# Kernel optimization log

Measured on AMD Instinct MI355X. Metric: run time of the kernel, lower is better.

## Reference

```python
import jax, jax.numpy as jnp
import numpy as np

SAMPLE_RATE = 44100
NUM_FILTERS = 3
FREQ_LO, FREQ_HI = 100.0, 3000.0
Q_LO, Q_HI = 1.0, 5.0
GAIN_LO, GAIN_HI = -24.0, 24.0


def _center_freqs():
    # power_ratio(i/N, f_lo, f_hi) = f_lo * (f_hi/f_lo)**(i/N)
    return [FREQ_LO * (FREQ_HI / FREQ_LO) ** (i / NUM_FILTERS) for i in range(NUM_FILTERS)]


def setup_inputs() -> dict:
    key = jax.random.key(0)
    k1, k2, k3 = jax.random.split(key, 3)
    audio = jax.random.normal(k1, (32, 441000), dtype=jnp.float32)  # [B, T]
    # Q sampled like power_ratio(u, q_lo, q_hi) = q_lo*(q_hi/q_lo)**u
    u = jax.random.uniform(k2, (NUM_FILTERS,), dtype=jnp.float32)
    qs = Q_LO * (Q_HI / Q_LO) ** u
    gains = jax.random.uniform(k3, (NUM_FILTERS,), dtype=jnp.float32,
                               minval=GAIN_LO, maxval=GAIN_HI)
    return {"audio": audio, "qs": qs, "gains": gains}


def _biquad(x, b0, b1, b2, a1, a2):
    """Direct-form-I biquad over time axis. x: [B, T]; coeffs normalized by a0."""
    B = x.shape[0]
    z = jnp.zeros((B,), x.dtype)

    def step(carry, xn):
        x1, x2, y1, y2 = carry
        yn = b0 * xn + b1 * x1 + b2 * x2 - a1 * y1 - a2 * y2
        return (xn, x1, yn, y1), yn

    _, y = jax.lax.scan(step, (z, z, z, z), x.T)  # scan over T
    return y.T


def _peaking_eq(audio, center_freq, gain, Q):
    # torchaudio.functional.equalizer_biquad coefficients
    w0 = 2.0 * jnp.pi * center_freq / SAMPLE_RATE
    alpha = jnp.sin(w0) / (2.0 * Q)
    A = jnp.exp(gain / 40.0 * jnp.log(10.0))  # 10**(gain/40)
    b0 = 1.0 + alpha * A
    b1 = -2.0 * jnp.cos(w0)
    b2 = 1.0 - alpha * A
    a0 = 1.0 + alpha / A
    a1 = -2.0 * jnp.cos(w0)
    a2 = 1.0 - alpha / A
    return _biquad(audio, b0 / a0, b1 / a0, b2 / a0, a1 / a0, a2 / a0)


def reference(audio, qs, gains):
    cfs = _center_freqs()
    for i in range(NUM_FILTERS):
        audio = _peaking_eq(audio, cfs[i], gains[i], qs[i])
    return audio
```

## Files before the change

### kernel.cpp

```cpp
#include <hip/hip_runtime.h>
#include <math.h>

#define SR      44100.0
#define T_LEN   441000
#define B_ROWS  32
#define NCH     13782
#define GCH     (B_ROWS * NCH)
#define WPR     216
#define NWAVE   (B_ROWS * WPR)
#define NBLK    (NWAVE / 4)
#define NSEG    8
#define SEGCH   1724
#define ROUNDS  10

#define WS_MAT  0
#define WS_T    512
#define WS_F    4096

typedef __attribute__((address_space(1))) const void gconst_t;
typedef __attribute__((address_space(3))) void lds_t;
#define GL2LDS(gp, lp) __builtin_amdgcn_global_load_lds((gconst_t*)(gp), (lds_t*)(lp), 16, 0, 0)


#define COMPUTE_COEFS_TO_LDS(scoef, qs, gains) do { \
    if (threadIdx.x < 3) { \
      int f = threadIdx.x; \
      double cfq = 100.0 * exp(log(30.0) * (double)f / 3.0); \
      double w0 = 2.0 * M_PI * cfq / SR; \
      double alpha = sin(w0) / (2.0 * (double)qs[f]); \
      double Ag = exp((double)gains[f] * (2.302585092994045684 / 40.0)); \
      double a0 = 1.0 + alpha / Ag; \
      scoef[f*5+0] = (float)((1.0 + alpha * Ag) / a0); \
      scoef[f*5+1] = (float)((-2.0 * cos(w0)) / a0); \
      scoef[f*5+2] = (float)((1.0 - alpha * Ag) / a0); \
      scoef[f*5+3] = (float)((-2.0 * cos(w0)) / a0); \
      scoef[f*5+4] = (float)((1.0 - alpha / Ag) / a0); \
    } \
  } while (0)

#define LOAD_COEFS(cf) \
  const float b00=cf[0],b10=cf[1],b20=cf[2],a10=cf[3],a20=cf[4]; \
  const float b01=cf[5],b11=cf[6],b21=cf[7],a11=cf[8],a21=cf[9]; \
  const float b02=cf[10],b12=cf[11],b22=cf[12],a12=cf[13],a22=cf[14];

#define CASCADE_STEP(xx) do { \
    float y1 = fmaf(b00, (xx), s11); \
    s11 = fmaf(-a10, y1, fmaf(b10, (xx), s21)); \
    s21 = fmaf(-a20, y1, b20 * (xx)); \
    float y2 = fmaf(b01, y1, s12); \
    s12 = fmaf(-a11, y2, fmaf(b11, y1, s22)); \
    s22 = fmaf(-a21, y2, b21 * y1); \
    y3 = fmaf(b02, y2, s13); \
    s13 = fmaf(-a12, y3, fmaf(b12, y2, s23)); \
    s23 = fmaf(-a22, y3, b22 * y2); \
  } while (0)

#define MV6(dst, M, v, add) do { \
    _Pragma("unroll") \
    for (int _i = 0; _i < 6; _i++) { \
      float _s = (add)[_i]; \
      _Pragma("unroll") \
      for (int _k = 0; _k < 6; _k++) _s = fmaf((M)[_i*6+_k], (v)[_k], _s); \
      (dst)[_i] = _s; \
    } \
  } while (0)

__device__ __forceinline__ void mm6d(const double* X, const double* Y, double* Z, int t) {
  if (t < 36) {
    int i = t / 6, j = t % 6;
    double s = 0.0;
    #pragma unroll
    for (int k = 0; k < 6; k++) s += X[i*6+k] * Y[k*6+j];
    Z[t] = s;
  }
}


__global__ __launch_bounds__(256) void kA_states(const float* __restrict__ x,
                                                 const float* __restrict__ qs,
                                                 const float* __restrict__ gains,
                                                 float* __restrict__ ws) {
  __shared__ float lds[4 * 2048];
  __shared__ float scoef[16];
  int wib = threadIdx.x >> 6, lane = threadIdx.x & 63;
  int gw = blockIdx.x * 4 + wib;
  int row = gw / WPR, wci = gw % WPR;
  long rowbase = (long)row * T_LEN;
  int s0 = wci << 11;
  int span4 = (min(2048, T_LEN - s0)) >> 2;
  const float4* xp = (const float4*)(x + rowbase + s0);
  float* slab = lds + (wib << 11);
  if (span4 == 512) {
    #pragma unroll
    for (int i = 0; i < 8; i++) {
      int s = (i << 6) + lane;
      int g = (s & ~7) | ((s & 7) ^ ((s >> 3) & 7));
      GL2LDS(xp + g, slab + (i << 8));
    }
  } else {
    #pragma unroll
    for (int i = 0; i < 8; i++) {
      int s = (i << 6) + lane;
      int g = (s & ~7) | ((s & 7) ^ ((s >> 3) & 7));
      if (g < span4) GL2LDS(xp + g, slab + (i << 8));
    }
  }
  COMPUTE_COEFS_TO_LDS(scoef, qs, gains);
  __syncthreads();
  int ci = (wci << 6) + lane;
  if (ci < NCH) {
    LOAD_COEFS(scoef);
    int rem = min(32, T_LEN - (ci << 5));
    int n4 = rem >> 2;
    const float* rowp = slab + (lane << 5);
    int xr = lane & 7;
    float s11=0,s21=0,s12=0,s22=0,s13=0,s23=0, y3;
    if (n4 == 8) {
      #pragma unroll
      for (int j4 = 0; j4 < 8; j4++) {
        float4 v = *(const float4*)(rowp + ((j4 ^ xr) << 2));
        CASCADE_STEP(v.x); CASCADE_STEP(v.y); CASCADE_STEP(v.z); CASCADE_STEP(v.w);
      }
    } else {
      for (int j4 = 0; j4 < n4; j4++) {
        float4 v = *(const float4*)(rowp + ((j4 ^ xr) << 2));
        CASCADE_STEP(v.x); CASCADE_STEP(v.y); CASCADE_STEP(v.z); CASCADE_STEP(v.w);
      }
    }
    (void)y3;
    float2* F = (float2*)(ws + WS_F + ((long)row * NCH + ci) * 6);
    F[0] = make_float2(s11, s21); F[1] = make_float2(s12, s22); F[2] = make_float2(s13, s23);
  }
}


__device__ __forceinline__ void scan_setup(const float* qs, const float* gains, int t,
                                           double* Da, double* Db, double* Dc, double* Dd,
                                           float* sW, float (*sV)[36], float* sG) {
  __shared__ double dco[3][5];
  if (t < 3) {
    int f = t;
    double cfq = 100.0 * exp(log(30.0) * (double)f / 3.0);
    double w0 = 2.0 * M_PI * cfq / SR;
    double alpha = sin(w0) / (2.0 * (double)qs[f]);
    double Ag = exp((double)gains[f] * (2.302585092994045684 / 40.0));
    double a0 = 1.0 + alpha / Ag;
    dco[f][0] = (1.0 + alpha * Ag) / a0;
    dco[f][1] = (-2.0 * cos(w0)) / a0;
    dco[f][2] = (1.0 - alpha * Ag) / a0;
    dco[f][3] = (-2.0 * cos(w0)) / a0;
    dco[f][4] = (1.0 - alpha / Ag) / a0;
  }
  __syncthreads();
  if (t == 0) {
    double u[7] = {0,0,0,0,0,0,1};
    for (int f = 0; f < 3; f++) {
      double b0=dco[f][0], b1=dco[f][1], b2=dco[f][2], a1=dco[f][3], a2=dco[f][4];
      double yv[7], s1p[7], s2p[7];
      for (int i = 0; i < 7; i++) {
        yv[i]  = b0 * u[i] + ((i == 2*f)   ? 1.0 : 0.0);
        s1p[i] = b1 * u[i] + ((i == 2*f+1) ? 1.0 : 0.0) - a1 * yv[i];
        s2p[i] = b2 * u[i] - a2 * yv[i];
      }
      for (int i = 0; i < 6; i++) { Da[(2*f)*6+i] = s1p[i]; Da[(2*f+1)*6+i] = s2p[i]; }
      for (int i = 0; i < 7; i++) u[i] = yv[i];
    }
  }
  if (t < 36) Dc[t] = (t % 7 == 0) ? 1.0 : 0.0;
  __syncthreads();
  mm6d(Da, Da, Db, t); __syncthreads();
  mm6d(Db, Db, Da, t); __syncthreads();
  mm6d(Da, Da, Db, t); __syncthreads();
  mm6d(Db, Db, Da, t); __syncthreads();
  mm6d(Da, Da, Db, t); __syncthreads();
  if (t < 36) sW[t] = (float)Db[t];
  mm6d(Db, Db, Da, t); __syncthreads();
  double* cur = Da; double* oth = Db;
  double* Gc = Dc; double* Gd = Dd;
  #pragma unroll
  for (int k = 0; k < ROUNDS; k++) {
    if (t < 36) sV[k][t] = (float)cur[t];
    if ((SEGCH >> (k + 1)) & 1) {
      __syncthreads();
      mm6d(Gc, cur, Gd, t); __syncthreads();
      double* tm = Gc; Gc = Gd; Gd = tm;
    }
    if (k < ROUNDS - 1) {
      __syncthreads();
      mm6d(cur, cur, oth, t); __syncthreads();
      double* tm = cur; cur = oth; oth = tm;
    }
  }
  if (t < 36) sG[t] = (float)Gc[t];
  __syncthreads();
}


__global__ __launch_bounds__(1024) void kB_scan(const float* __restrict__ qs,
                                                const float* __restrict__ gains,
                                                float* __restrict__ ws) {
  int seg = blockIdx.x & 7, row = blockIdx.x >> 3, t = threadIdx.x;
  __shared__ double Da[36], Db[36], Dc[36], Dd[36];
  __shared__ float sW[36], sV[ROUNDS][36], sG[36];
  __shared__ float bufA[1024][7], bufB[1024][7];
  scan_setup(qs, gains, t, Da, Db, Dc, Dd, sW, sV, sG);
  if (blockIdx.x == 0 && t < 36) {
    ws[WS_MAT + t] = sW[t];
    #pragma unroll
    for (int k = 0; k < ROUNDS; k++) ws[WS_MAT + (k + 1) * 36 + t] = sV[k][t];
    ws[WS_MAT + 11 * 36 + t] = sG[t];
  }
  int segstart = seg * SEGCH;
  int nch = min(SEGCH, NCH - segstart);
  int nact = nch >> 1;
  float* F = ws + WS_F + ((long)row * NCH + segstart) * 6;
  float v[6] = {0,0,0,0,0,0};
  float f0[6] = {0,0,0,0,0,0};
  if (t < nact) {
    const float4* Fp = (const float4*)(F + 12 * t);
    float4 l0 = Fp[0], l1 = Fp[1], l2 = Fp[2];
    f0[0]=l0.x; f0[1]=l0.y; f0[2]=l0.z; f0[3]=l0.w; f0[4]=l1.x; f0[5]=l1.y;
    float f1[6] = {l1.z, l1.w, l2.x, l2.y, l2.z, l2.w};
    MV6(v, sW, f0, f1);
  }
  #pragma unroll
  for (int i = 0; i < 6; i++) bufA[t][i] = v[i];
  __syncthreads();
  float (*src)[7] = bufA, (*dst)[7] = bufB;
  for (int k = 0; k < ROUNDS; k++) {
    int d = 1 << k;
    float nv[6];
    if (t >= d) { MV6(nv, sV[k], src[t-d], src[t]); }
    else {
      #pragma unroll
      for (int i = 0; i < 6; i++) nv[i] = src[t][i];
    }
    #pragma unroll
    for (int i = 0; i < 6; i++) dst[t][i] = nv[i];
    __syncthreads();
    float (*tm)[7] = src; src = dst; dst = tm;
  }
  if (t == nact - 1) {
    float* Tp = ws + WS_T + (long)blockIdx.x * 6;
    #pragma unroll
    for (int i = 0; i < 6; i++) Tp[i] = src[t][i];
  }
  if (t < nact) {
    float e[6];
    if (t > 0) {
      #pragma unroll
      for (int i = 0; i < 6; i++) e[i] = src[t-1][i];
    } else {
      #pragma unroll
      for (int i = 0; i < 6; i++) e[i] = 0.0f;
    }
    float e1[6];
    MV6(e1, sW, e, f0);
    float4* Fp = (float4*)(F + 12 * t);
    Fp[0] = make_float4(e[0], e[1], e[2], e[3]);
    Fp[1] = make_float4(e[4], e[5], e1[0], e1[1]);
    Fp[2] = make_float4(e1[2], e1[3], e1[4], e1[5]);
  }
}


__global__ __launch_bounds__(256) void kC_emit(const float* __restrict__ x,
                                               const float* __restrict__ qs,
                                               const float* __restrict__ gains,
                                               float* __restrict__ y,
                                               const float* __restrict__ ws) {
  __shared__ float lds[4 * 2048];
  __shared__ float scoef[16];
  __shared__ float smat[432];
  __shared__ float sTT[96];
  __shared__ float sO[96];
  int tid = threadIdx.x;
  int wib = tid >> 6, lane = tid & 63;
  int gw = blockIdx.x * 4 + wib;
  int row = gw / WPR, wci = gw % WPR;
  int rowA = (blockIdx.x * 4) / WPR;
  long rowbase = (long)row * T_LEN;
  int s0 = wci << 11;
  int span4 = (min(2048, T_LEN - s0)) >> 2;
  const float4* xp = (const float4*)(x + rowbase + s0);
  float* slab = lds + (wib << 11);
  if (span4 == 512) {
    #pragma unroll
    for (int i = 0; i < 8; i++) {
      int s = (i << 6) + lane;
      int g = (s & ~7) | ((s & 7) ^ ((s >> 3) & 7));
      GL2LDS(xp + g, slab + (i << 8));
    }
  } else {
    #pragma unroll
    for (int i = 0; i < 8; i++) {
      int s = (i << 6) + lane;
      int g = (s & ~7) | ((s & 7) ^ ((s >> 3) & 7));
      if (g < span4) GL2LDS(xp + g, slab + (i << 8));
    }
  }
  for (int i = tid; i < 432; i += 256) smat[i] = ws[WS_MAT + i];
  {
    int rowB = (blockIdx.x * 4 + 3) / WPR;
    if (tid < 96) {
      int r = (tid < 48) ? rowA : rowB;
      int j = tid - ((tid < 48) ? 0 : 48);
      sTT[tid] = ws[WS_T + (long)r * 48 + j];
    }
  }
  COMPUTE_COEFS_TO_LDS(scoef, qs, gains);
  int ci = (wci << 6) + lane;
  float e0=0,e1v=0,e2=0,e3=0,e4=0,e5=0;
  if (ci < NCH) {
    const float2* E = (const float2*)(ws + WS_F + ((long)row * NCH + ci) * 6);
    float2 p0 = E[0], p1 = E[1], p2 = E[2];
    e0=p0.x; e1v=p0.y; e2=p1.x; e3=p1.y; e4=p2.x; e5=p2.y;
  }
  __syncthreads();
  if (tid < 16) {
    int rsel = tid >> 3, sg = tid & 7;
    const float* Gm = smat + 11 * 36;
    float o[6] = {0,0,0,0,0,0};
    for (int s2 = 0; s2 < sg; s2++) {
      float no[6];
      MV6(no, Gm, o, &sTT[rsel * 48 + s2 * 6]);
      #pragma unroll
      for (int i = 0; i < 6; i++) o[i] = no[i];
    }
    #pragma unroll
    for (int i = 0; i < 6; i++) sO[tid * 6 + i] = o[i];
  }
  __syncthreads();
  if (ci < NCH) {
    LOAD_COEFS(scoef);
    int seg = ci / SEGCH;
    int d = ci - seg * SEGCH;
    int rsel = (row == rowA) ? 0 : 1;
    const float* op = sO + (rsel * 8 + seg) * 6;
    float m[6];
    #pragma unroll
    for (int i = 0; i < 6; i++) m[i] = op[i];
    float z6[6] = {0,0,0,0,0,0};
    #pragma unroll
    for (int k = 0; k < 11; k++) {
      if ((d >> k) & 1) {
        float nm[6];
        MV6(nm, smat + k * 36, m, z6);
        #pragma unroll
        for (int i = 0; i < 6; i++) m[i] = nm[i];
      }
    }
    float s11=e0+m[0], s21=e1v+m[1], s12=e2+m[2], s22=e3+m[3], s13=e4+m[4], s23=e5+m[5];
    int rem = min(32, T_LEN - (ci << 5));
    int n4 = rem >> 2;
    float* rowp = slab + (lane << 5);
    int xr = lane & 7;
    float y3;
    if (n4 == 8) {
      #pragma unroll
      for (int j4 = 0; j4 < 8; j4++) {
        float* p = rowp + ((j4 ^ xr) << 2);
        float4 v = *(const float4*)p;
        float4 o;
        CASCADE_STEP(v.x); o.x = y3;
        CASCADE_STEP(v.y); o.y = y3;
        CASCADE_STEP(v.z); o.z = y3;
        CASCADE_STEP(v.w); o.w = y3;
        *(float4*)p = o;
      }
    } else {
      for (int j4 = 0; j4 < n4; j4++) {
        float* p = rowp + ((j4 ^ xr) << 2);
        float4 v = *(const float4*)p;
        float4 o;
        CASCADE_STEP(v.x); o.x = y3;
        CASCADE_STEP(v.y); o.y = y3;
        CASCADE_STEP(v.z); o.z = y3;
        CASCADE_STEP(v.w); o.w = y3;
        *(float4*)p = o;
      }
    }
  }
  __syncthreads();
  float4* yp = (float4*)(y + rowbase + s0);
  if (span4 == 512) {
    #pragma unroll
    for (int i = 0; i < 8; i++) {
      int g = (i << 6) + lane;
      int s = (g & ~7) | ((g & 7) ^ ((g >> 3) & 7));
      yp[g] = *(const float4*)(slab + (s << 2));
    }
  } else {
    #pragma unroll
    for (int i = 0; i < 8; i++) {
      int g = (i << 6) + lane;
      int s = (g & ~7) | ((g & 7) ^ ((g >> 3) & 7));
      if (g < span4) yp[g] = *(const float4*)(slab + (s << 2));
    }
  }
}

extern "C" void kernel_launch(void* const* d_in, const int* in_sizes, int n_in,
                              void* d_out, int out_size, void* d_ws, size_t ws_size,
                              hipStream_t stream) {
  const float* audio = (const float*)d_in[0];
  const float* qs    = (const float*)d_in[1];
  const float* gains = (const float*)d_in[2];
  float* out = (float*)d_out;
  float* ws  = (float*)d_ws;

  hipLaunchKernelGGL(kA_states, dim3(NBLK), dim3(256), 0, stream, audio, qs, gains, ws);
  hipLaunchKernelGGL(kB_scan, dim3(B_ROWS * NSEG), dim3(1024), 0, stream, qs, gains, ws);
  hipLaunchKernelGGL(kC_emit, dim3(NBLK), dim3(256), 0, stream, audio, qs, gains, out, ws);
}
```

Measured before the change: 68.08 us.

## Fuse intra-block state scan into first kernel, shrink middle scan to per-block offsets

The first kernel now computes the transition-matrix powers itself and runs a 256-chunk Kogge-Stone scan of per-chunk states in LDS, writing exclusive prefixes plus block aggregates. The middle kernel shrinks from 256 blocks of 1024 threads scanning 8 segments per row to 32 tiny blocks scanning 54 block aggregates. The emit kernel then applies only a block offset and up to 8 matrix powers instead of a serial segment chain and 11 powers. This is meant to cut the heavy middle launch and its global state traffic. In exchange, every first-kernel block redoes the double-precision matrix squaring and adds several barriers.

```diff
diff --git a/kernel.cpp b/kernel.cpp
--- a/kernel.cpp
+++ b/kernel.cpp
@@ -6,23 +6,21 @@
 #define B_ROWS  32
 #define NCH     13782
 #define GCH     (B_ROWS * NCH)
-#define WPR     216
-#define NWAVE   (B_ROWS * WPR)
-#define NBLK    (NWAVE / 4)
-#define NSEG    8
-#define SEGCH   1724
-#define ROUNDS  10
+#define BPR     54
+#define NBLK    (B_ROWS * BPR)
+#define NMAT    14
 
 #define WS_MAT  0
-#define WS_T    512
-#define WS_F    4096
+#define WS_AG   512
+#define WS_O    10880
+#define WS_F    21248
 
 typedef __attribute__((address_space(1))) const void gconst_t;
 typedef __attribute__((address_space(3))) void lds_t;
 #define GL2LDS(gp, lp) __builtin_amdgcn_global_load_lds((gconst_t*)(gp), (lds_t*)(lp), 16, 0, 0)
 
 
-#define COMPUTE_COEFS_TO_LDS(scoef, qs, gains) do { \
+#define COMPUTE_COEFS(scoef, dco, qs, gains) do { \
     if (threadIdx.x < 3) { \
       int f = threadIdx.x; \
       double cfq = 100.0 * exp(log(30.0) * (double)f / 3.0); \
@@ -30,11 +28,15 @@
       double alpha = sin(w0) / (2.0 * (double)qs[f]); \
       double Ag = exp((double)gains[f] * (2.302585092994045684 / 40.0)); \
       double a0 = 1.0 + alpha / Ag; \
-      scoef[f*5+0] = (float)((1.0 + alpha * Ag) / a0); \
-      scoef[f*5+1] = (float)((-2.0 * cos(w0)) / a0); \
-      scoef[f*5+2] = (float)((1.0 - alpha * Ag) / a0); \
-      scoef[f*5+3] = (float)((-2.0 * cos(w0)) / a0); \
-      scoef[f*5+4] = (float)((1.0 - alpha / Ag) / a0); \
+      double c0 = (1.0 + alpha * Ag) / a0; \
+      double c1 = (-2.0 * cos(w0)) / a0; \
+      double c2 = (1.0 - alpha * Ag) / a0; \
+      double c3 = c1; \
+      double c4 = (1.0 - alpha / Ag) / a0; \
+      if (dco) { double* dc = (double*)(dco); \
+        dc[f*5+0]=c0; dc[f*5+1]=c1; dc[f*5+2]=c2; dc[f*5+3]=c3; dc[f*5+4]=c4; } \
+      scoef[f*5+0]=(float)c0; scoef[f*5+1]=(float)c1; scoef[f*5+2]=(float)c2; \
+      scoef[f*5+3]=(float)c3; scoef[f*5+4]=(float)c4; \
     } \
   } while (0)
 
@@ -76,15 +78,21 @@
 }
 
 
-__global__ __launch_bounds__(256) void kA_states(const float* __restrict__ x,
-                                                 const float* __restrict__ qs,
-                                                 const float* __restrict__ gains,
-                                                 float* __restrict__ ws) {
-  __shared__ float lds[4 * 2048];
+
+__global__ __launch_bounds__(256) void kA_scan(const float* __restrict__ x,
+                                               const float* __restrict__ qs,
+                                               const float* __restrict__ gains,
+                                               float* __restrict__ ws) {
+  __shared__ __align__(16) float lds[4 * 2048];
+  __shared__ double Da[36], Db[36];
+  __shared__ double dco[15];
+  __shared__ float sVm[NMAT][36];
   __shared__ float scoef[16];
-  int wib = threadIdx.x >> 6, lane = threadIdx.x & 63;
-  int gw = blockIdx.x * 4 + wib;
-  int row = gw / WPR, wci = gw % WPR;
+  const int tid = threadIdx.x;
+  const int wib = tid >> 6, lane = tid & 63;
+  const int b = blockIdx.x;
+  const int row = b / BPR, jb = b - row * BPR;
+  const int wci = (jb << 2) + wib;
   long rowbase = (long)row * T_LEN;
   int s0 = wci << 11;
   int span4 = (min(2048, T_LEN - s0)) >> 2;
@@ -105,10 +113,47 @@
       if (g < span4) GL2LDS(xp + g, slab + (i << 8));
     }
   }
-  COMPUTE_COEFS_TO_LDS(scoef, qs, gains);
-  __syncthreads();
-  int ci = (wci << 6) + lane;
-  if (ci < NCH) {
+  COMPUTE_COEFS(scoef, dco, qs, gains);
+  if (wib == 0) {
+    if (lane == 0) {
+      double u[7] = {0,0,0,0,0,0,1};
+      for (int f = 0; f < 3; f++) {
+        double c0=dco[f*5+0], c1=dco[f*5+1], c2=dco[f*5+2], c3=dco[f*5+3], c4=dco[f*5+4];
+        double yv[7], s1p[7], s2p[7];
+        for (int i = 0; i < 7; i++) {
+          yv[i]  = c0 * u[i] + ((i == 2*f)   ? 1.0 : 0.0);
+          s1p[i] = c1 * u[i] + ((i == 2*f+1) ? 1.0 : 0.0) - c3 * yv[i];
+          s2p[i] = c2 * u[i] - c4 * yv[i];
+        }
+        for (int i = 0; i < 6; i++) { Da[(2*f)*6+i] = s1p[i]; Da[(2*f+1)*6+i] = s2p[i]; }
+        for (int i = 0; i < 7; i++) u[i] = yv[i];
+      }
+    }
+    double* cur = Da; double* oth = Db;
+    #pragma unroll
+    for (int s = 0; s < 5; s++) {
+      mm6d(cur, cur, oth, lane);
+      double* tm = cur; cur = oth; oth = tm;
+    }
+    #pragma unroll
+    for (int k = 0; k < NMAT; k++) {
+      if (lane < 36) {
+        float wv = (float)cur[lane];
+        sVm[k][lane] = wv;
+        if (b == 0) ws[WS_MAT + k*36 + lane] = wv;
+      }
+      if (k < NMAT - 1) {
+        mm6d(cur, cur, oth, lane);
+        double* tm = cur; cur = oth; oth = tm;
+      }
+    }
+  }
+  __syncthreads();
+
+  int ci = (jb << 8) + tid;
+  bool valid = ci < NCH;
+  float f[6] = {0,0,0,0,0,0};
+  if (valid) {
     LOAD_COEFS(scoef);
     int rem = min(32, T_LEN - (ci << 5));
     int n4 = rem >> 2;
@@ -128,138 +173,86 @@
       }
     }
     (void)y3;
-    float2* F = (float2*)(ws + WS_F + ((long)row * NCH + ci) * 6);
-    F[0] = make_float2(s11, s21); F[1] = make_float2(s12, s22); F[2] = make_float2(s13, s23);
-  }
-}
-
-
-__device__ __forceinline__ void scan_setup(const float* qs, const float* gains, int t,
-                                           double* Da, double* Db, double* Dc, double* Dd,
-                                           float* sW, float (*sV)[36], float* sG) {
-  __shared__ double dco[3][5];
-  if (t < 3) {
-    int f = t;
-    double cfq = 100.0 * exp(log(30.0) * (double)f / 3.0);
-    double w0 = 2.0 * M_PI * cfq / SR;
-    double alpha = sin(w0) / (2.0 * (double)qs[f]);
-    double Ag = exp((double)gains[f] * (2.302585092994045684 / 40.0));
-    double a0 = 1.0 + alpha / Ag;
-    dco[f][0] = (1.0 + alpha * Ag) / a0;
-    dco[f][1] = (-2.0 * cos(w0)) / a0;
-    dco[f][2] = (1.0 - alpha * Ag) / a0;
-    dco[f][3] = (-2.0 * cos(w0)) / a0;
-    dco[f][4] = (1.0 - alpha / Ag) / a0;
-  }
-  __syncthreads();
-  if (t == 0) {
-    double u[7] = {0,0,0,0,0,0,1};
-    for (int f = 0; f < 3; f++) {
-      double b0=dco[f][0], b1=dco[f][1], b2=dco[f][2], a1=dco[f][3], a2=dco[f][4];
-      double yv[7], s1p[7], s2p[7];
-      for (int i = 0; i < 7; i++) {
-        yv[i]  = b0 * u[i] + ((i == 2*f)   ? 1.0 : 0.0);
-        s1p[i] = b1 * u[i] + ((i == 2*f+1) ? 1.0 : 0.0) - a1 * yv[i];
-        s2p[i] = b2 * u[i] - a2 * yv[i];
-      }
-      for (int i = 0; i < 6; i++) { Da[(2*f)*6+i] = s1p[i]; Da[(2*f+1)*6+i] = s2p[i]; }
-      for (int i = 0; i < 7; i++) u[i] = yv[i];
-    }
-  }
-  if (t < 36) Dc[t] = (t % 7 == 0) ? 1.0 : 0.0;
-  __syncthreads();
-  mm6d(Da, Da, Db, t); __syncthreads();
-  mm6d(Db, Db, Da, t); __syncthreads();
-  mm6d(Da, Da, Db, t); __syncthreads();
-  mm6d(Db, Db, Da, t); __syncthreads();
-  mm6d(Da, Da, Db, t); __syncthreads();
-  if (t < 36) sW[t] = (float)Db[t];
-  mm6d(Db, Db, Da, t); __syncthreads();
-  double* cur = Da; double* oth = Db;
-  double* Gc = Dc; double* Gd = Dd;
+    f[0]=s11; f[1]=s21; f[2]=s12; f[3]=s22; f[4]=s13; f[5]=s23;
+  }
+  __syncthreads();
+
+  float* src = lds;
+  float* dst = lds + 1792;
   #pragma unroll
-  for (int k = 0; k < ROUNDS; k++) {
-    if (t < 36) sV[k][t] = (float)cur[t];
-    if ((SEGCH >> (k + 1)) & 1) {
-      __syncthreads();
-      mm6d(Gc, cur, Gd, t); __syncthreads();
-      double* tm = Gc; Gc = Gd; Gd = tm;
-    }
-    if (k < ROUNDS - 1) {
-      __syncthreads();
-      mm6d(cur, cur, oth, t); __syncthreads();
-      double* tm = cur; cur = oth; oth = tm;
-    }
-  }
-  if (t < 36) sG[t] = (float)Gc[t];
-  __syncthreads();
-}
-
-
-__global__ __launch_bounds__(1024) void kB_scan(const float* __restrict__ qs,
-                                                const float* __restrict__ gains,
-                                                float* __restrict__ ws) {
-  int seg = blockIdx.x & 7, row = blockIdx.x >> 3, t = threadIdx.x;
-  __shared__ double Da[36], Db[36], Dc[36], Dd[36];
-  __shared__ float sW[36], sV[ROUNDS][36], sG[36];
-  __shared__ float bufA[1024][7], bufB[1024][7];
-  scan_setup(qs, gains, t, Da, Db, Dc, Dd, sW, sV, sG);
-  if (blockIdx.x == 0 && t < 36) {
-    ws[WS_MAT + t] = sW[t];
-    #pragma unroll
-    for (int k = 0; k < ROUNDS; k++) ws[WS_MAT + (k + 1) * 36 + t] = sV[k][t];
-    ws[WS_MAT + 11 * 36 + t] = sG[t];
-  }
-  int segstart = seg * SEGCH;
-  int nch = min(SEGCH, NCH - segstart);
-  int nact = nch >> 1;
-  float* F = ws + WS_F + ((long)row * NCH + segstart) * 6;
-  float v[6] = {0,0,0,0,0,0};
-  float f0[6] = {0,0,0,0,0,0};
-  if (t < nact) {
-    const float4* Fp = (const float4*)(F + 12 * t);
-    float4 l0 = Fp[0], l1 = Fp[1], l2 = Fp[2];
-    f0[0]=l0.x; f0[1]=l0.y; f0[2]=l0.z; f0[3]=l0.w; f0[4]=l1.x; f0[5]=l1.y;
-    float f1[6] = {l1.z, l1.w, l2.x, l2.y, l2.z, l2.w};
-    MV6(v, sW, f0, f1);
-  }
-  #pragma unroll
-  for (int i = 0; i < 6; i++) bufA[t][i] = v[i];
-  __syncthreads();
-  float (*src)[7] = bufA, (*dst)[7] = bufB;
-  for (int k = 0; k < ROUNDS; k++) {
+  for (int i = 0; i < 6; i++) src[tid*7 + i] = f[i];
+  __syncthreads();
+  for (int k = 0; k < 8; k++) {
     int d = 1 << k;
     float nv[6];
-    if (t >= d) { MV6(nv, sV[k], src[t-d], src[t]); }
+    if (tid >= d) { MV6(nv, sVm[k], src + (tid-d)*7, src + tid*7); }
     else {
       #pragma unroll
-      for (int i = 0; i < 6; i++) nv[i] = src[t][i];
-    }
-    #pragma unroll
-    for (int i = 0; i < 6; i++) dst[t][i] = nv[i];
+      for (int i = 0; i < 6; i++) nv[i] = src[tid*7 + i];
+    }
+    #pragma unroll
+    for (int i = 0; i < 6; i++) dst[tid*7 + i] = nv[i];
     __syncthreads();
-    float (*tm)[7] = src; src = dst; dst = tm;
-  }
-  if (t == nact - 1) {
-    float* Tp = ws + WS_T + (long)blockIdx.x * 6;
-    #pragma unroll
-    for (int i = 0; i < 6; i++) Tp[i] = src[t][i];
-  }
-  if (t < nact) {
+    float* tm = src; src = dst; dst = tm;
+  }
+  if (valid) {
     float e[6];
-    if (t > 0) {
-      #pragma unroll
-      for (int i = 0; i < 6; i++) e[i] = src[t-1][i];
+    if (tid > 0) {
+      #pragma unroll
+      for (int i = 0; i < 6; i++) e[i] = src[(tid-1)*7 + i];
     } else {
       #pragma unroll
       for (int i = 0; i < 6; i++) e[i] = 0.0f;
     }
-    float e1[6];
-    MV6(e1, sW, e, f0);
-    float4* Fp = (float4*)(F + 12 * t);
-    Fp[0] = make_float4(e[0], e[1], e[2], e[3]);
-    Fp[1] = make_float4(e[4], e[5], e1[0], e1[1]);
-    Fp[2] = make_float4(e1[2], e1[3], e1[4], e1[5]);
+    float2* E = (float2*)(ws + WS_F + ((long)row * NCH + ci) * 6);
+    E[0] = make_float2(e[0], e[1]); E[1] = make_float2(e[2], e[3]); E[2] = make_float2(e[4], e[5]);
+  }
+  if (tid == 255 && jb < BPR - 1) {
+    #pragma unroll
+    for (int i = 0; i < 6; i++) ws[WS_AG + ((long)row * BPR + jb) * 6 + i] = src[255*7 + i];
+  }
+}
+
+
+__global__ __launch_bounds__(64) void kB_off(float* __restrict__ ws) {
+  int row = blockIdx.x, j = threadIdx.x;
+  __shared__ float sB[6][36];
+  __shared__ float buf[2][64][7];
+  for (int i = j; i < 216; i += 64) sB[i/36][i%36] = ws[WS_MAT + (8 + i/36)*36 + (i%36)];
+  float v[6] = {0,0,0,0,0,0};
+  if (j < BPR - 1) {
+    #pragma unroll
+    for (int i = 0; i < 6; i++) v[i] = ws[WS_AG + ((long)row * BPR + j) * 6 + i];
+  }
+  __syncthreads();
+  #pragma unroll
+  for (int i = 0; i < 6; i++) buf[0][j][i] = v[i];
+  __syncthreads();
+  int cur = 0;
+  for (int k = 0; k < 6; k++) {
+    int d = 1 << k;
+    float nv[6];
+    if (j >= d) { MV6(nv, sB[k], buf[cur][j-d], buf[cur][j]); }
+    else {
+      #pragma unroll
+      for (int i = 0; i < 6; i++) nv[i] = buf[cur][j][i];
+    }
+    #pragma unroll
+    for (int i = 0; i < 6; i++) buf[cur^1][j][i] = nv[i];
+    __syncthreads();
+    cur ^= 1;
+  }
+  if (j < BPR) {
+    float o[6];
+    if (j > 0) {
+      #pragma unroll
+      for (int i = 0; i < 6; i++) o[i] = buf[cur][j-1][i];
+    } else {
+      #pragma unroll
+      for (int i = 0; i < 6; i++) o[i] = 0.0f;
+    }
+    #pragma unroll
+    for (int i = 0; i < 6; i++) ws[WS_O + ((long)row * BPR + j) * 6 + i] = o[i];
   }
 }
 
@@ -269,16 +262,14 @@
                                                const float* __restrict__ gains,
                                                float* __restrict__ y,
                                                const float* __restrict__ ws) {
-  __shared__ float lds[4 * 2048];
+  __shared__ __align__(16) float lds[4 * 2048];
   __shared__ float scoef[16];
-  __shared__ float smat[432];
-  __shared__ float sTT[96];
-  __shared__ float sO[96];
-  int tid = threadIdx.x;
-  int wib = tid >> 6, lane = tid & 63;
-  int gw = blockIdx.x * 4 + wib;
-  int row = gw / WPR, wci = gw % WPR;
-  int rowA = (blockIdx.x * 4) / WPR;
+  __shared__ float smat[288];
+  const int tid = threadIdx.x;
+  const int wib = tid >> 6, lane = tid & 63;
+  const int b = blockIdx.x;
+  const int row = b / BPR, jb = b - row * BPR;
+  const int wci = (jb << 2) + wib;
   long rowbase = (long)row * T_LEN;
   int s0 = wci << 11;
   int span4 = (min(2048, T_LEN - s0)) >> 2;
@@ -299,53 +290,34 @@
       if (g < span4) GL2LDS(xp + g, slab + (i << 8));
     }
   }
-  for (int i = tid; i < 432; i += 256) smat[i] = ws[WS_MAT + i];
+  for (int i = tid; i < 288; i += 256) smat[i] = ws[WS_MAT + i];
+  COMPUTE_COEFS(scoef, (double*)nullptr, qs, gains);
+  float o6[6];
   {
-    int rowB = (blockIdx.x * 4 + 3) / WPR;
-    if (tid < 96) {
-      int r = (tid < 48) ? rowA : rowB;
-      int j = tid - ((tid < 48) ? 0 : 48);
-      sTT[tid] = ws[WS_T + (long)r * 48 + j];
-    }
-  }
-  COMPUTE_COEFS_TO_LDS(scoef, qs, gains);
-  int ci = (wci << 6) + lane;
+    const float* Op = ws + WS_O + ((long)row * BPR + jb) * 6;
+    #pragma unroll
+    for (int i = 0; i < 6; i++) o6[i] = Op[i];
+  }
+  int ci = (jb << 8) + tid;
+  bool valid = ci < NCH;
   float e0=0,e1v=0,e2=0,e3=0,e4=0,e5=0;
-  if (ci < NCH) {
+  if (valid) {
     const float2* E = (const float2*)(ws + WS_F + ((long)row * NCH + ci) * 6);
     float2 p0 = E[0], p1 = E[1], p2 = E[2];
     e0=p0.x; e1v=p0.y; e2=p1.x; e3=p1.y; e4=p2.x; e5=p2.y;
   }
   __syncthreads();
-  if (tid < 16) {
-    int rsel = tid >> 3, sg = tid & 7;
-    const float* Gm = smat + 11 * 36;
-    float o[6] = {0,0,0,0,0,0};
-    for (int s2 = 0; s2 < sg; s2++) {
-      float no[6];
-      MV6(no, Gm, o, &sTT[rsel * 48 + s2 * 6]);
-      #pragma unroll
-      for (int i = 0; i < 6; i++) o[i] = no[i];
-    }
-    #pragma unroll
-    for (int i = 0; i < 6; i++) sO[tid * 6 + i] = o[i];
-  }
-  __syncthreads();
-  if (ci < NCH) {
+  if (valid) {
     LOAD_COEFS(scoef);
-    int seg = ci / SEGCH;
-    int d = ci - seg * SEGCH;
-    int rsel = (row == rowA) ? 0 : 1;
-    const float* op = sO + (rsel * 8 + seg) * 6;
     float m[6];
     #pragma unroll
-    for (int i = 0; i < 6; i++) m[i] = op[i];
+    for (int i = 0; i < 6; i++) m[i] = o6[i];
     float z6[6] = {0,0,0,0,0,0};
     #pragma unroll
-    for (int k = 0; k < 11; k++) {
-      if ((d >> k) & 1) {
+    for (int k = 0; k < 8; k++) {
+      if ((tid >> k) & 1) {
         float nm[6];
-        MV6(nm, smat + k * 36, m, z6);
+        MV6(nm, smat + k*36, m, z6);
         #pragma unroll
         for (int i = 0; i < 6; i++) m[i] = nm[i];
       }
@@ -409,7 +381,7 @@
   float* out = (float*)d_out;
   float* ws  = (float*)d_ws;
 
-  hipLaunchKernelGGL(kA_states, dim3(NBLK), dim3(256), 0, stream, audio, qs, gains, ws);
-  hipLaunchKernelGGL(kB_scan, dim3(B_ROWS * NSEG), dim3(1024), 0, stream, qs, gains, ws);
+  hipLaunchKernelGGL(kA_scan, dim3(NBLK), dim3(256), 0, stream, audio, qs, gains, ws);
+  hipLaunchKernelGGL(kB_off, dim3(B_ROWS), dim3(64), 0, stream, ws);
   hipLaunchKernelGGL(kC_emit, dim3(NBLK), dim3(256), 0, stream, audio, qs, gains, out, ws);
 }
```

Result: faster. 62.61 us (-8.0%).
